# Kernel optimization log

Measured on AMD Instinct MI355X. Metric: run time of the kernel, lower is better.

The kernel has to match this reference:

```python
import jax, jax.numpy as jnp
import numpy as np

BIN_SIZE = 256
TOP_K = 16


def setup_inputs() -> dict:
    key = jax.random.key(0)
    kx, kc = jax.random.split(key)
    x = jax.random.normal(kx, (2, 4096, 512), dtype=jnp.float32)
    codebook = jax.random.normal(kc, (512, 16), dtype=jnp.float32)  # (feature_dim, max_num_bins//2)
    return {"x": x, "codebook": codebook}


def reference(x, codebook):
    B, N, F = x.shape
    n_bins = N // BIN_SIZE  # 16
    # LSH bucket assignment: project onto random hyperplanes, pick argmax of [p, -p]
    mul = x @ codebook[:, : n_bins // 2]                      # (B, N, n_bins//2)
    cmul = jnp.concatenate([mul, -mul], axis=-1)              # (B, N, n_bins)
    bin_idx = jnp.argmax(cmul, axis=-1)                       # (B, N)
    # argsort-based binning: equal-size bins of points sorted by bucket id
    bins_split = jnp.argsort(bin_idx, axis=-1).reshape(B, n_bins, BIN_SIZE)
    # gather points into bins: (B, n_bins, bin_size, F)
    points_binned = jnp.take_along_axis(x[:, None, :, :], bins_split[..., None], axis=2)
    # intra-bin dense similarity + sigmoid
    dm = jax.nn.sigmoid(jnp.einsum('bnif,bnjf->bnij', points_binned, points_binned))
    vals, idx = jax.lax.top_k(dm, TOP_K)                      # (B, n_bins, bin_size, k)
    # map local bin indices back to global point indices
    dst = jnp.take_along_axis(bins_split[:, :, None, :], idx, axis=-1)  # (B, nb, bs, k)
    src = jnp.broadcast_to(bins_split[..., None], dst.shape)
    b = jnp.broadcast_to(jnp.arange(B)[:, None, None, None], dst.shape)
    # dense equivalent of the coalesced batched sparse_coo_tensor of size (N, N)
    out = jnp.zeros((B, N, N), dtype=x.dtype).at[b, src, dst].add(vals)
    return out
```

## Files before the change

kernel.cpp:

```cpp
#include <hip/hip_runtime.h>
#include <stdint.h>
#include <math.h>

#define NPTS 4096
#define NF 512
#define NBINS 16
#define BSZ 256
#define TOPK 16
#define NBATCH 2
#define SPART (NBATCH * NBINS * BSZ * BSZ)

typedef float vf4 __attribute__((ext_vector_type(4)));

__global__ __launch_bounds__(256) void k_assign(const float* __restrict__ x,
                                                const float* __restrict__ cb,
                                                int* __restrict__ bin_idx) {
    int gw   = (blockIdx.x * 256 + threadIdx.x) >> 6;
    int lane = threadIdx.x & 63;
    const float* row = x + (size_t)gw * NF;
    float acc[8];
#pragma unroll
    for (int j = 0; j < 8; j++) acc[j] = 0.f;
    for (int f = lane; f < NF; f += 64) {
        float xv = row[f];
        const float4* c = (const float4*)(cb + f * 16);
        float4 c0 = c[0], c1 = c[1];
        acc[0] += xv * c0.x; acc[1] += xv * c0.y; acc[2] += xv * c0.z; acc[3] += xv * c0.w;
        acc[4] += xv * c1.x; acc[5] += xv * c1.y; acc[6] += xv * c1.z; acc[7] += xv * c1.w;
    }
#pragma unroll
    for (int off = 32; off > 0; off >>= 1) {
#pragma unroll
        for (int j = 0; j < 8; j++) acc[j] += __shfl_xor(acc[j], off, 64);
    }
    if (lane == 0) {
        float best = acc[0]; int bi = 0;
#pragma unroll
        for (int j = 1; j < 8; j++) { if (acc[j] > best) { best = acc[j]; bi = j; } }
#pragma unroll
        for (int j = 0; j < 8; j++) { float v = -acc[j]; if (v > best) { best = v; bi = 8 + j; } }
        bin_idx[gw] = bi;
    }
}

__global__ __launch_bounds__(256) void k_sort(const int* __restrict__ bin_idx,
                                              int* __restrict__ order) {
    __shared__ int hist[NBINS][256];
    __shared__ int segsum[NBINS][16];
    __shared__ int segoff[NBINS][16];
    __shared__ int totals[NBINS];
    __shared__ int keybase[NBINS];
    int b = blockIdx.x, t = threadIdx.x;
    const int* bi = bin_idx + b * NPTS;
#pragma unroll
    for (int j = 0; j < NBINS; j++) hist[j][t] = 0;
    int base = t * 16;
    for (int i = 0; i < 16; i++) { int k = bi[base + i]; hist[k][t]++; }
    __syncthreads();
    {
        int j = t >> 4, sg = t & 15, s = 0;
#pragma unroll
        for (int u = 0; u < 16; u++) s += hist[j][sg * 16 + u];
        segsum[j][sg] = s;
    }
    __syncthreads();
    if (t < NBINS) {
        int run = 0;
#pragma unroll
        for (int sg = 0; sg < 16; sg++) { int c = segsum[t][sg]; segoff[t][sg] = run; run += c; }
        totals[t] = run;
    }
    __syncthreads();
    if (t == 0) {
        int run = 0;
#pragma unroll
        for (int j = 0; j < NBINS; j++) { keybase[j] = run; run += totals[j]; }
    }
    __syncthreads();
    {
        int j = t >> 4, sg = t & 15;
        int run = segoff[j][sg];
#pragma unroll
        for (int u = 0; u < 16; u++) { int c = hist[j][sg * 16 + u]; hist[j][sg * 16 + u] = run; run += c; }
    }
    __syncthreads();
    int* ob = order + b * NPTS;
    for (int i = 0; i < 16; i++) {
        int k = bi[base + i];
        int o = hist[k][t];
        hist[k][t] = o + 1;
        ob[keybase[k] + o] = base + i;
    }
}

__global__ __launch_bounds__(256, 2) void k_gemm(const float* __restrict__ x,
                                                 const int* __restrict__ order,
                                                 float* __restrict__ S) {
    int blk = blockIdx.x;
    int kh  = blk & 3;
    int tn  = (blk >> 2) & 1;
    int tm  = (blk >> 3) & 1;
    int bin = (blk >> 4) & 15;
    int b   = blk >> 8;
    int t  = threadIdx.x;
    int tx = t & 15, ty = t >> 4;
    __shared__ int   idxA[128];
    __shared__ int   idxB[128];
    __shared__ float Asl[32][132];
    __shared__ float Bsl[32][132];
    int ob = b * NPTS + bin * BSZ;
    if (t < 128) idxA[t] = order[ob + tm * 128 + t];
    else         idxB[t - 128] = order[ob + tn * 128 + (t - 128)];
    __syncthreads();
    const float* xb = x + (size_t)b * (NPTS * NF);
    int rowi = t & 127;
    int qb   = t >> 7;
    const float* rowA = xb + (size_t)idxA[rowi] * NF + kh * 128;
    const float* rowB = xb + (size_t)idxB[rowi] * NF + kh * 128;
    float acc[8][8];
#pragma unroll
    for (int i = 0; i < 8; i++)
#pragma unroll
        for (int j = 0; j < 8; j++) acc[i][j] = 0.f;
    float4 pa[4], pb[4];
#pragma unroll
    for (int l = 0; l < 4; l++) {
        pa[l] = *(const float4*)(rowA + (qb + 2 * l) * 4);
        pb[l] = *(const float4*)(rowB + (qb + 2 * l) * 4);
    }
    for (int it = 0; it < 4; it++) {
        __syncthreads();
#pragma unroll
        for (int l = 0; l < 4; l++) {
            int kq = (qb + 2 * l) * 4;
            Asl[kq + 0][rowi] = pa[l].x; Asl[kq + 1][rowi] = pa[l].y;
            Asl[kq + 2][rowi] = pa[l].z; Asl[kq + 3][rowi] = pa[l].w;
            Bsl[kq + 0][rowi] = pb[l].x; Bsl[kq + 1][rowi] = pb[l].y;
            Bsl[kq + 2][rowi] = pb[l].z; Bsl[kq + 3][rowi] = pb[l].w;
        }
        __syncthreads();
        if (it < 3) {
            const float* a2 = rowA + (it + 1) * 32;
            const float* b2 = rowB + (it + 1) * 32;
#pragma unroll
            for (int l = 0; l < 4; l++) {
                pa[l] = *(const float4*)(a2 + (qb + 2 * l) * 4);
                pb[l] = *(const float4*)(b2 + (qb + 2 * l) * 4);
            }
        }
#pragma unroll
        for (int kk = 0; kk < 32; kk++) {
            float4 a0 = *(const float4*)&Asl[kk][ty * 8];
            float4 a1 = *(const float4*)&Asl[kk][ty * 8 + 4];
            float4 b0 = *(const float4*)&Bsl[kk][tx * 8];
            float4 b1 = *(const float4*)&Bsl[kk][tx * 8 + 4];
            float av[8] = {a0.x, a0.y, a0.z, a0.w, a1.x, a1.y, a1.z, a1.w};
            float bv[8] = {b0.x, b0.y, b0.z, b0.w, b1.x, b1.y, b1.z, b1.w};
#pragma unroll
            for (int i = 0; i < 8; i++)
#pragma unroll
                for (int j = 0; j < 8; j++) acc[i][j] += av[i] * bv[j];
        }
    }
    float* Sp = S + (size_t)kh * SPART;
    size_t rowbase = (size_t)(b * NBINS + bin) * BSZ;
#pragma unroll
    for (int i = 0; i < 8; i++) {
        int r = tm * 128 + ty * 8 + i;
        float* orow = Sp + (rowbase + r) * BSZ + tn * 128 + tx * 8;
        *(float4*)(orow)     = make_float4(acc[i][0], acc[i][1], acc[i][2], acc[i][3]);
        *(float4*)(orow + 4) = make_float4(acc[i][4], acc[i][5], acc[i][6], acc[i][7]);
    }
}

__global__ __launch_bounds__(64) void k_topkw(const float* __restrict__ S,
                                              const int* __restrict__ order,
                                              float* __restrict__ out) {
    __shared__ float buf[NPTS];
    int row  = blockIdx.x;
    int lane = threadIdx.x;
    const float* s0 = S + (size_t)row * BSZ;
    unsigned long long key[4];
#pragma unroll
    for (int q = 0; q < 4; q++) {
        int j = lane + 64 * q;
        float d = s0[j] + s0[j + SPART] + s0[j + 2 * SPART] + s0[j + 3 * SPART];
        float v = 1.0f / (1.0f + expf(-d));
        key[q] = ((unsigned long long)__float_as_uint(v) << 32) | (unsigned)(255 - j);
    }
    int   wj[TOPK];
    float wv[TOPK];
#pragma unroll
    for (int it = 0; it < TOPK; it++) {
        unsigned long long k = key[0];
        if (key[1] > k) k = key[1];
        if (key[2] > k) k = key[2];
        if (key[3] > k) k = key[3];
#pragma unroll
        for (int off = 32; off > 0; off >>= 1) {
            unsigned long long o = __shfl_xor(k, off, 64);
            if (o > k) k = o;
        }
        int jw = 255 - (int)(k & 0xFFull);
        wj[it] = jw;
        wv[it] = __uint_as_float((unsigned)(k >> 32));
        if ((jw & 63) == lane) {
            int q = jw >> 6;
            if      (q == 0) key[0] = 0ull;
            else if (q == 1) key[1] = 0ull;
            else if (q == 2) key[2] = 0ull;
            else             key[3] = 0ull;
        }
    }
    vf4 z = {0.f, 0.f, 0.f, 0.f};
#pragma unroll
    for (int u = 0; u < 16; u++) ((vf4*)buf)[u * 64 + lane] = z;
    int b   = row >> 12;
    int bin = (row >> 8) & 15;
    int i   = row & 255;
    const int* obp = order + b * NPTS + bin * BSZ;
    int srcg = obp[i];
    __syncthreads();
#pragma unroll
    for (int it = 0; it < TOPK; it++) {
        if (lane == it) buf[obp[wj[it]]] = wv[it];
    }
    __syncthreads();
    vf4* orow = (vf4*)(out + ((size_t)b * NPTS + srcg) * NPTS);
#pragma unroll
    for (int u = 0; u < 16; u++) {
        __builtin_nontemporal_store(((const vf4*)buf)[u * 64 + lane], &orow[u * 64 + lane]);
    }
}

extern "C" void kernel_launch(void* const* d_in, const int* in_sizes, int n_in,
                              void* d_out, int out_size, void* d_ws, size_t ws_size,
                              hipStream_t stream) {
    const float* x  = (const float*)d_in[0];
    const float* cb = (const float*)d_in[1];
    float* out = (float*)d_out;
    int*   bin_idx = (int*)d_ws;
    int*   order   = bin_idx + NBATCH * NPTS;
    float* S       = (float*)d_ws + 4 * NBATCH * NPTS;

    k_assign<<<2048, 256, 0, stream>>>(x, cb, bin_idx);
    k_sort  <<<NBATCH, 256, 0, stream>>>(bin_idx, order);
    k_gemm  <<<512, 256, 0, stream>>>(x, order, S);
    k_topkw <<<NBATCH * NPTS * NBINS / 16, 64, 0, stream>>>(S, order, out);
}
```

Measured before the change: 213.3 us.

## Widen sort to 1024 threads and drop LDS staging in top-k writer

The counting sort now runs 1024 threads per batch, with each thread loading four keys via an int4 and computing the per-bin prefix with wave shuffles instead of a serial segment scan. The top-k/write kernel packs four rows per 256-thread block and drops the shared-memory row buffer and its barriers. Each lane now builds its output vectors directly by matching against the 16 winner columns held in registers. This removes the sort's serial latency and the LDS traffic and syncs in the writer, in exchange for 16 compares per stored vector and a global order lookup inside the selection loop.

```diff
diff --git a/kernel.cpp b/kernel.cpp
--- a/kernel.cpp
+++ b/kernel.cpp
@@ -43,54 +43,47 @@
     }
 }
 
-__global__ __launch_bounds__(256) void k_sort(const int* __restrict__ bin_idx,
-                                              int* __restrict__ order) {
-    __shared__ int hist[NBINS][256];
-    __shared__ int segsum[NBINS][16];
-    __shared__ int segoff[NBINS][16];
+__global__ __launch_bounds__(1024) void k_sort(const int* __restrict__ bin_idx,
+                                               int* __restrict__ order) {
+    __shared__ int hist[NBINS][1024];
     __shared__ int totals[NBINS];
     __shared__ int keybase[NBINS];
     int b = blockIdx.x, t = threadIdx.x;
+    int w = t >> 6, lane = t & 63;
     const int* bi = bin_idx + b * NPTS;
 #pragma unroll
     for (int j = 0; j < NBINS; j++) hist[j][t] = 0;
-    int base = t * 16;
-    for (int i = 0; i < 16; i++) { int k = bi[base + i]; hist[k][t]++; }
-    __syncthreads();
-    {
-        int j = t >> 4, sg = t & 15, s = 0;
-#pragma unroll
-        for (int u = 0; u < 16; u++) s += hist[j][sg * 16 + u];
-        segsum[j][sg] = s;
-    }
-    __syncthreads();
-    if (t < NBINS) {
-        int run = 0;
-#pragma unroll
-        for (int sg = 0; sg < 16; sg++) { int c = segsum[t][sg]; segoff[t][sg] = run; run += c; }
-        totals[t] = run;
-    }
+    int4 kk = *(const int4*)(bi + t * 4);
+    int k0 = kk.x, k1 = kk.y, k2 = kk.z, k3 = kk.w;
+    hist[k0][t]++; hist[k1][t]++; hist[k2][t]++; hist[k3][t]++;
+    __syncthreads();
+    int base = lane * 16;
+    int s = 0;
+#pragma unroll
+    for (int u = 0; u < 16; u++) s += hist[w][base + u];
+    int incl = s;
+#pragma unroll
+    for (int off = 1; off < 64; off <<= 1) {
+        int n = __shfl_up(incl, off, 64);
+        if (lane >= off) incl += n;
+    }
+    int excl = incl - s;
+    if (lane == 63) totals[w] = incl;
     __syncthreads();
     if (t == 0) {
         int run = 0;
 #pragma unroll
         for (int j = 0; j < NBINS; j++) { keybase[j] = run; run += totals[j]; }
     }
-    __syncthreads();
-    {
-        int j = t >> 4, sg = t & 15;
-        int run = segoff[j][sg];
-#pragma unroll
-        for (int u = 0; u < 16; u++) { int c = hist[j][sg * 16 + u]; hist[j][sg * 16 + u] = run; run += c; }
-    }
+    int run = excl;
+#pragma unroll
+    for (int u = 0; u < 16; u++) { int c = hist[w][base + u]; hist[w][base + u] = run; run += c; }
     __syncthreads();
     int* ob = order + b * NPTS;
-    for (int i = 0; i < 16; i++) {
-        int k = bi[base + i];
-        int o = hist[k][t];
-        hist[k][t] = o + 1;
-        ob[keybase[k] + o] = base + i;
-    }
+    int o0 = hist[k0][t]; hist[k0][t] = o0 + 1; ob[keybase[k0] + o0] = t * 4 + 0;
+    int o1 = hist[k1][t]; hist[k1][t] = o1 + 1; ob[keybase[k1] + o1] = t * 4 + 1;
+    int o2 = hist[k2][t]; hist[k2][t] = o2 + 1; ob[keybase[k2] + o2] = t * 4 + 2;
+    int o3 = hist[k3][t]; hist[k3][t] = o3 + 1; ob[keybase[k3] + o3] = t * 4 + 3;
 }
 
 __global__ __launch_bounds__(256, 2) void k_gemm(const float* __restrict__ x,
@@ -173,12 +166,11 @@
     }
 }
 
-__global__ __launch_bounds__(64) void k_topkw(const float* __restrict__ S,
-                                              const int* __restrict__ order,
-                                              float* __restrict__ out) {
-    __shared__ float buf[NPTS];
-    int row  = blockIdx.x;
-    int lane = threadIdx.x;
+__global__ __launch_bounds__(256) void k_topkw(const float* __restrict__ S,
+                                               const int* __restrict__ order,
+                                               float* __restrict__ out) {
+    int lane = threadIdx.x & 63;
+    int row  = blockIdx.x * 4 + (threadIdx.x >> 6);
     const float* s0 = S + (size_t)row * BSZ;
     unsigned long long key[4];
 #pragma unroll
@@ -188,7 +180,11 @@
         float v = 1.0f / (1.0f + expf(-d));
         key[q] = ((unsigned long long)__float_as_uint(v) << 32) | (unsigned)(255 - j);
     }
-    int   wj[TOPK];
+    int b   = row >> 12;
+    int bin = (row >> 8) & 15;
+    int i   = row & 255;
+    const int* obp = order + b * NPTS + bin * BSZ;
+    int   wg[TOPK];
     float wv[TOPK];
 #pragma unroll
     for (int it = 0; it < TOPK; it++) {
@@ -202,8 +198,8 @@
             if (o > k) k = o;
         }
         int jw = 255 - (int)(k & 0xFFull);
-        wj[it] = jw;
         wv[it] = __uint_as_float((unsigned)(k >> 32));
+        wg[it] = obp[__builtin_amdgcn_readfirstlane(jw)];
         if ((jw & 63) == lane) {
             int q = jw >> 6;
             if      (q == 0) key[0] = 0ull;
@@ -212,24 +208,23 @@
             else             key[3] = 0ull;
         }
     }
-    vf4 z = {0.f, 0.f, 0.f, 0.f};
-#pragma unroll
-    for (int u = 0; u < 16; u++) ((vf4*)buf)[u * 64 + lane] = z;
-    int b   = row >> 12;
-    int bin = (row >> 8) & 15;
-    int i   = row & 255;
-    const int* obp = order + b * NPTS + bin * BSZ;
     int srcg = obp[i];
-    __syncthreads();
-#pragma unroll
-    for (int it = 0; it < TOPK; it++) {
-        if (lane == it) buf[obp[wj[it]]] = wv[it];
-    }
-    __syncthreads();
     vf4* orow = (vf4*)(out + ((size_t)b * NPTS + srcg) * NPTS);
 #pragma unroll
     for (int u = 0; u < 16; u++) {
-        __builtin_nontemporal_store(((const vf4*)buf)[u * 64 + lane], &orow[u * 64 + lane]);
+        vf4 v = {0.f, 0.f, 0.f, 0.f};
+        int colbase = u * 256 + lane * 4;
+#pragma unroll
+        for (int it = 0; it < TOPK; it++) {
+            if ((wg[it] & ~3) == colbase) {
+                int c = wg[it] & 3;
+                if      (c == 0) v.x = wv[it];
+                else if (c == 1) v.y = wv[it];
+                else if (c == 2) v.z = wv[it];
+                else             v.w = wv[it];
+            }
+        }
+        __builtin_nontemporal_store(v, &orow[u * 64 + lane]);
     }
 }
 
@@ -244,7 +239,7 @@
     float* S       = (float*)d_ws + 4 * NBATCH * NPTS;
 
     k_assign<<<2048, 256, 0, stream>>>(x, cb, bin_idx);
-    k_sort  <<<NBATCH, 256, 0, stream>>>(bin_idx, order);
+    k_sort  <<<NBATCH, 1024, 0, stream>>>(bin_idx, order);
     k_gemm  <<<512, 256, 0, stream>>>(x, order, S);
-    k_topkw <<<NBATCH * NPTS * NBINS / 16, 64, 0, stream>>>(S, order, out);
-}
+    k_topkw <<<2048, 256, 0, stream>>>(S, order, out);
+}
```

New measurement: 212.2 us. About the same (-0.5%).
